# Kernel tuning notes

Measured on AMD Instinct MI355X. Metric: run time of the kernel, lower is better.

Reference implementation:

```python
import jax, jax.numpy as jnp
import numpy as np

N = 100000   # nodes
E = 1600000  # edges
IN, HID, OUT = 128, 128, 64


def setup_inputs() -> dict:
    key = jax.random.key(0)
    ks = jax.random.split(key, 8)
    x = jax.random.normal(ks[0], (N, IN), dtype=jnp.float32)
    edge_index = jax.random.randint(ks[1], (2, E), 0, N, dtype=jnp.int64)
    W1 = jax.random.normal(ks[2], (IN, HID), dtype=jnp.float32) * 0.05
    b1 = jnp.zeros((HID,), dtype=jnp.float32)
    W2 = jax.random.normal(ks[3], (HID, OUT), dtype=jnp.float32) * 0.05
    b2 = jnp.zeros((OUT,), dtype=jnp.float32)
    Wd = jax.random.normal(ks[4], (OUT, IN), dtype=jnp.float32) * 0.05
    bd = jnp.zeros((IN,), dtype=jnp.float32)
    return {"x": x, "edge_index": edge_index, "W1": W1, "b1": b1,
            "W2": W2, "b2": b2, "Wd": Wd, "bd": bd}


def _gcn_conv(x, src, dst, W, b):
    # PyG GCNConv: add self-loops, symmetric normalization D^-1/2 (A+I) D^-1/2,
    # messages flow src -> dst, aggregated by sum at dst.
    h = x @ W                                   # [N, F]
    ones = jnp.ones((src.shape[0],), x.dtype)
    deg = jax.ops.segment_sum(ones, dst, num_segments=N) + 1.0  # +1 for self-loop
    dinv = jax.lax.rsqrt(deg)                   # deg^-1/2, [N]
    coef = dinv[src] * dinv[dst]                # per-edge norm
    agg = jax.ops.segment_sum(h[src] * coef[:, None], dst, num_segments=N)
    agg = agg + h * (dinv * dinv)[:, None]      # self-loop contribution
    return agg + b


def reference(x, edge_index, W1, b1, W2, b2, Wd, bd):
    src, dst = edge_index[0], edge_index[1]
    h = jax.nn.relu(_gcn_conv(x, src, dst, W1, b1))
    # dropout in eval mode -> identity
    z = _gcn_conv(h, src, dst, W2, b2)          # [N, OUT] embedding
    x_recon = z @ Wd + bd                        # [N, IN]
    return (x_recon, z)
```

## Files before the change

### kernel.cpp

```cpp
#include <hip/hip_runtime.h>
#include <hip/hip_bf16.h>
#include <hip/hip_fp16.h>


#define TPB 256
#define CAP 64

typedef float v2f __attribute__((ext_vector_type(2)));


__device__ __forceinline__ unsigned short f2bf(float f) {
    unsigned u = __float_as_uint(f);
    unsigned r = u + 0x7fffu + ((u >> 16) & 1u);
    return (unsigned short)(r >> 16);
}
__device__ __forceinline__ float bf_lo(unsigned u) { return __uint_as_float(u << 16); }
__device__ __forceinline__ float bf_hi(unsigned u) { return __uint_as_float(u & 0xffff0000u); }


template <int K, int C, int TN, bool BIAS, bool INBF, bool OUTBF>
__device__ __forceinline__ void gemm_body(const void* __restrict__ Ap,
                                          const float* __restrict__ W,
                                          const float* __restrict__ bias,
                                          void* __restrict__ outp, int N, int bid,
                                          float* __restrict__ Ws) {
    constexpr int BM  = 128;
    constexpr int TM  = 8;
    constexpr int BK  = 32;
    constexpr int NCT = C / TN;
    static_assert(NCT * (BM / TM) == TPB, "thread layout");

    int tid = threadIdx.x;
    int tc = tid % NCT;
    int tr = tid / NCT;
    int c0 = tc * TN;
    int r0 = bid * BM + tr * TM;

    float acc[TM][TN] = {};

    for (int k0 = 0; k0 < K; k0 += BK) {
        __syncthreads();
        for (int i = tid * 4; i < BK * C; i += TPB * 4)
            *(float4*)&Ws[i] = *(const float4*)&W[k0 * C + i];
        __syncthreads();

        for (int k = 0; k < BK; k += 4) {
            float4 a[TM];
            uint2  au[TM];
#pragma unroll
            for (int i = 0; i < TM; ++i) {
                int r = r0 + i;
                if (r >= N) r = N - 1;
                if (INBF)
                    au[i] = *(const uint2*)((const unsigned short*)Ap + (size_t)r * K + k0 + k);
                else
                    a[i] = *(const float4*)((const float*)Ap + (size_t)r * K + k0 + k);
            }
#pragma unroll
            for (int kk = 0; kk < 4; ++kk) {
                float w[TN];
#pragma unroll
                for (int j = 0; j < TN; j += 4)
                    *(float4*)&w[j] = *(const float4*)&Ws[(k + kk) * C + c0 + j];
#pragma unroll
                for (int i = 0; i < TM; ++i) {
                    float av;
                    if (INBF) {
                        unsigned uu = (kk < 2) ? au[i].x : au[i].y;
                        av = (kk & 1) ? bf_hi(uu) : bf_lo(uu);
                    } else {
                        av = ((const float*)&a[i])[kk];
                    }
#pragma unroll
                    for (int j = 0; j < TN; ++j) acc[i][j] += av * w[j];
                }
            }
        }
    }

#pragma unroll
    for (int i = 0; i < TM; ++i) {
        int r = r0 + i;
        if (r >= N) continue;
        if (BIAS) {
#pragma unroll
            for (int j = 0; j < TN; ++j) acc[i][j] += bias[c0 + j];
        }
        if (OUTBF) {
            unsigned short* ob = (unsigned short*)outp + (size_t)r * C + c0;
            unsigned pk[TN / 2];
#pragma unroll
            for (int j = 0; j < TN; j += 2)
                pk[j / 2] = (unsigned)f2bf(acc[i][j]) | ((unsigned)f2bf(acc[i][j + 1]) << 16);
            if (TN == 8)      *(uint4*)ob = *(uint4*)pk;
            else if (TN == 4) *(uint2*)ob = *(uint2*)pk;
        } else {
            float* of = (float*)outp + (size_t)r * C + c0;
#pragma unroll
            for (int j = 0; j < TN; j += 4)
                *(float4*)&of[j] = *(float4*)&acc[i][j];
        }
    }
}

template <int K, int C, int TN, bool BIAS, bool INBF, bool OUTBF>
__global__ __launch_bounds__(TPB) void gemm_k(const void* __restrict__ Ap,
                                              const float* __restrict__ W,
                                              const float* __restrict__ bias,
                                              void* __restrict__ outp, int N) {
    __shared__ float Ws[32 * C];
    gemm_body<K, C, TN, BIAS, INBF, OUTBF>(Ap, W, bias, outp, N, blockIdx.x, Ws);
}


__global__ __launch_bounds__(TPB) void fused1_k(const float* __restrict__ x,
                                                const float* __restrict__ W1,
                                                unsigned* __restrict__ h1b,
                                                const int* __restrict__ src,
                                                const int* __restrict__ dst,
                                                int* __restrict__ cnt,
                                                unsigned* __restrict__ bucket,
                                                int N, int E, int gb) {
    __shared__ float Ws[32 * 128];
    if ((int)blockIdx.x < gb) {
        gemm_body<128, 128, 8, false, false, true>(x, W1, nullptr, h1b, N, blockIdx.x, Ws);
    } else {
        int bid = (int)blockIdx.x - gb;
        int e0 = (bid * TPB + (int)threadIdx.x) * 8;
        if (e0 + 7 < E) {
            int4 sa = *(const int4*)&src[e0];
            int4 sb = *(const int4*)&src[e0 + 4];
            int4 da = *(const int4*)&dst[e0];
            int4 db = *(const int4*)&dst[e0 + 4];
            int ss[8] = {sa.x, sa.y, sa.z, sa.w, sb.x, sb.y, sb.z, sb.w};
            int dd[8] = {da.x, da.y, da.z, da.w, db.x, db.y, db.z, db.w};
            int rr[8];
#pragma unroll
            for (int q = 0; q < 8; ++q) rr[q] = atomicAdd(&cnt[dd[q]], 1);
#pragma unroll
            for (int q = 0; q < 8; ++q)
                if (rr[q] < CAP) bucket[(size_t)rr[q] * N + dd[q]] = (unsigned)ss[q];
        } else {
            for (int e = e0; e < E; ++e) {
                int s = src[e], d = dst[e];
                int r = atomicAdd(&cnt[d], 1);
                if (r < CAP) bucket[(size_t)r * N + d] = (unsigned)s;
            }
        }
    }
}


template <int F2, bool RELU, bool OUTBF>
__global__ __launch_bounds__(TPB) void agg_k(const unsigned* __restrict__ h,
                                             const int* __restrict__ cnt,
                                             const unsigned* __restrict__ bucket,
                                             const float* __restrict__ bias,
                                             void* __restrict__ outp, int N) {
    constexpr int NPB = TPB / F2;
    int ln = threadIdx.x / F2;
    int f2 = threadIdx.x % F2;
    int n  = blockIdx.x * NPB + ln;
    if (n >= N) return;

    int cfull = cnt[n];
    float di = rsqrtf((float)cfull + 1.0f);
    unsigned us = h[(size_t)n * F2 + f2];
    float ax = bf_lo(us) * (di * di);
    float ay = bf_hi(us) * (di * di);

    int cn = cfull < CAP ? cfull : CAP;
    const unsigned* bp = bucket + n;

    int j = 0;
    for (; j + 7 < cn; j += 8) {
        int s[8], cs[8];
        unsigned v[8];
#pragma unroll
        for (int q = 0; q < 8; ++q) s[q] = (int)bp[(size_t)(j + q) * N];
#pragma unroll
        for (int q = 0; q < 8; ++q) {
            v[q]  = h[(size_t)s[q] * F2 + f2];
            cs[q] = cnt[s[q]];
        }
#pragma unroll
        for (int q = 0; q < 8; ++q) {
            float c = rsqrtf((float)cs[q] + 1.0f) * di;
            ax += c * bf_lo(v[q]);
            ay += c * bf_hi(v[q]);
        }
    }
    for (; j < cn; ++j) {
        int s = (int)bp[(size_t)j * N];
        unsigned v = h[(size_t)s * F2 + f2];
        float c = rsqrtf((float)cnt[s] + 1.0f) * di;
        ax += c * bf_lo(v);
        ay += c * bf_hi(v);
    }

    float rx = ax + bias[2 * f2];
    float ry = ay + bias[2 * f2 + 1];
    if (RELU) { rx = fmaxf(rx, 0.f); ry = fmaxf(ry, 0.f); }
    if (OUTBF) {
        unsigned pk = (unsigned)f2bf(rx) | ((unsigned)f2bf(ry) << 16);
        ((unsigned*)outp)[(size_t)n * F2 + f2] = pk;
    } else {
        v2f r; r.x = rx; r.y = ry;
        __builtin_nontemporal_store(r, (v2f*)outp + (size_t)n * F2 + f2);
    }
}


extern "C" void kernel_launch(void* const* d_in, const int* in_sizes, int n_in,
                              void* d_out, int out_size, void* d_ws, size_t ws_size,
                              hipStream_t stream) {
    const float* x    = (const float*)d_in[0];
    const int*   eidx = (const int*)d_in[1];
    const float* W1   = (const float*)d_in[2];
    const float* b1   = (const float*)d_in[3];
    const float* W2   = (const float*)d_in[4];
    const float* b2   = (const float*)d_in[5];
    const float* Wd   = (const float*)d_in[6];
    const float* bd   = (const float*)d_in[7];

    const int N = in_sizes[0] / 128;
    const int E = in_sizes[1] / 2;
    const int* src = eidx;
    const int* dst = eidx + E;

    size_t off = 0;
    auto alloc = [&](size_t bytes) {
        void* p = (char*)d_ws + off;
        off += (bytes + 255) & ~(size_t)255;
        return p;
    };
    int*      cnt     = (int*)alloc((size_t)N * 4);
    unsigned* bucket  = (unsigned*)alloc((size_t)N * CAP * 4);
    unsigned* h1b     = (unsigned*)alloc((size_t)N * 64 * 4);
    unsigned* h2b     = (unsigned*)alloc((size_t)N * 32 * 4);
    unsigned* hrelu_b = (unsigned*)alloc((size_t)N * 64 * 4);
    (void)ws_size;

    float* x_recon = (float*)d_out;
    float* z_out   = (float*)d_out + (size_t)N * 128;

    const int gb = (N + 127) / 128;
    const int fb = (E + TPB * 8 - 1) / (TPB * 8);

    (void)hipMemsetAsync(cnt, 0, (size_t)N * 4, stream);

    fused1_k<<<gb + fb, TPB, 0, stream>>>(x, W1, h1b, src, dst, cnt, bucket, N, E, gb);

    agg_k<64, true, true><<<(N + 3) / 4, TPB, 0, stream>>>(h1b, cnt, bucket, b1, hrelu_b, N);
    gemm_k<128, 64, 4, false, true, true><<<gb, TPB, 0, stream>>>(hrelu_b, W2, nullptr, h2b, N);
    agg_k<32, false, false><<<(N + 7) / 8, TPB, 0, stream>>>(h2b, cnt, bucket, b2, z_out, N);
    gemm_k<64, 128, 8, true, false, false><<<gb, TPB, 0, stream>>>(z_out, Wd, bd, x_recon, N);
}
```

Before: 475.1 us.

## Pre-partition edges into destination-range bins before bucket fill

Edges are first binned into 8 destination-range bins, using a block-local histogram and one global atomic per bin, and written to a scratch buffer that reuses the hrelu workspace. A new fill kernel then walks each bin and does the cnt atomics and bucket scatter, so concurrent writes from a bin land in a narrower address range. The aim is better cache locality for the atomic counters and scattered bucket writes. It costs an extra kernel launch and a write and read of the binned edge list, and bins are capped at BINCAP, so edges could be dropped if a bin overflows.

```diff
diff --git a/kernel.cpp b/kernel.cpp
--- a/kernel.cpp
+++ b/kernel.cpp
@@ -5,6 +5,8 @@
 
 #define TPB 256
 #define CAP 64
+#define BINCAP 220000
+#define FILLW 112
 
 typedef float v2f __attribute__((ext_vector_type(2)));
 
@@ -118,33 +120,82 @@
                                                 unsigned* __restrict__ h1b,
                                                 const int* __restrict__ src,
                                                 const int* __restrict__ dst,
-                                                int* __restrict__ cnt,
-                                                unsigned* __restrict__ bucket,
-                                                int N, int E, int gb) {
+                                                uint2* __restrict__ binBuf,
+                                                int* __restrict__ binCnt,
+                                                int N, int E, int gb, unsigned M) {
     __shared__ float Ws[32 * 128];
+    __shared__ int hist[8], gbase[8], lpos[8];
     if ((int)blockIdx.x < gb) {
         gemm_body<128, 128, 8, false, false, true>(x, W1, nullptr, h1b, N, blockIdx.x, Ws);
     } else {
         int bid = (int)blockIdx.x - gb;
-        int e0 = (bid * TPB + (int)threadIdx.x) * 8;
-        if (e0 + 7 < E) {
+        int tid = (int)threadIdx.x;
+        if (tid < 8) { hist[tid] = 0; lpos[tid] = 0; }
+        __syncthreads();
+
+        int e0 = (bid * TPB + tid) * 8;
+        int ne = E - e0; ne = ne > 8 ? 8 : (ne < 0 ? 0 : ne);
+        int ss[8], dd[8], bb8[8];
+        if (ne == 8) {
             int4 sa = *(const int4*)&src[e0];
             int4 sb = *(const int4*)&src[e0 + 4];
             int4 da = *(const int4*)&dst[e0];
             int4 db = *(const int4*)&dst[e0 + 4];
-            int ss[8] = {sa.x, sa.y, sa.z, sa.w, sb.x, sb.y, sb.z, sb.w};
-            int dd[8] = {da.x, da.y, da.z, da.w, db.x, db.y, db.z, db.w};
+            ss[0]=sa.x; ss[1]=sa.y; ss[2]=sa.z; ss[3]=sa.w;
+            ss[4]=sb.x; ss[5]=sb.y; ss[6]=sb.z; ss[7]=sb.w;
+            dd[0]=da.x; dd[1]=da.y; dd[2]=da.z; dd[3]=da.w;
+            dd[4]=db.x; dd[5]=db.y; dd[6]=db.z; dd[7]=db.w;
+        } else {
+            for (int q = 0; q < ne; ++q) { ss[q] = src[e0 + q]; dd[q] = dst[e0 + q]; }
+        }
+        for (int q = 0; q < ne; ++q) {
+            bb8[q] = (int)(((unsigned long long)(unsigned)dd[q] * M) >> 32);
+            atomicAdd(&hist[bb8[q]], 1);
+        }
+        __syncthreads();
+        if (tid < 8) gbase[tid] = atomicAdd(&binCnt[tid], hist[tid]);
+        __syncthreads();
+        for (int q = 0; q < ne; ++q) {
+            int b = bb8[q];
+            int p = gbase[b] + atomicAdd(&lpos[b], 1);
+            if (p < BINCAP)
+                binBuf[(size_t)b * BINCAP + p] = make_uint2((unsigned)ss[q], (unsigned)dd[q]);
+        }
+    }
+}
+
+
+__global__ __launch_bounds__(TPB) void fill_k(const uint2* __restrict__ binBuf,
+                                              const int* __restrict__ binCnt,
+                                              int* __restrict__ cnt,
+                                              unsigned* __restrict__ bucket, int N) {
+    int bin = (int)blockIdx.x & 7;
+    int w   = (int)blockIdx.x >> 3;
+    int cb  = binCnt[bin];
+    if (cb > BINCAP) cb = BINCAP;
+    const uint2* eb = binBuf + (size_t)bin * BINCAP;
+
+    for (int base = w * (TPB * 8); base < cb; base += FILLW * (TPB * 8)) {
+        int e0 = base + (int)threadIdx.x * 8;
+        if (e0 + 8 <= cb) {
+            unsigned s[8], d[8];
+#pragma unroll
+            for (int q = 0; q < 8; q += 2) {
+                uint4 t = *(const uint4*)&eb[e0 + q];
+                s[q] = t.x; d[q] = t.y; s[q + 1] = t.z; d[q + 1] = t.w;
+            }
             int rr[8];
 #pragma unroll
-            for (int q = 0; q < 8; ++q) rr[q] = atomicAdd(&cnt[dd[q]], 1);
+            for (int q = 0; q < 8; ++q) rr[q] = atomicAdd(&cnt[(int)d[q]], 1);
 #pragma unroll
             for (int q = 0; q < 8; ++q)
-                if (rr[q] < CAP) bucket[(size_t)rr[q] * N + dd[q]] = (unsigned)ss[q];
+                if (rr[q] < CAP) bucket[(size_t)rr[q] * N + d[q]] = s[q];
         } else {
-            for (int e = e0; e < E; ++e) {
-                int s = src[e], d = dst[e];
-                int r = atomicAdd(&cnt[d], 1);
-                if (r < CAP) bucket[(size_t)r * N + d] = (unsigned)s;
+            int lim = e0 + 8 < cb ? e0 + 8 : cb;
+            for (int e = e0; e < lim; ++e) {
+                uint2 t = eb[e];
+                int r = atomicAdd(&cnt[(int)t.y], 1);
+                if (r < CAP) bucket[(size_t)r * N + t.y] = t.x;
             }
         }
     }
@@ -239,17 +290,22 @@
     unsigned* h1b     = (unsigned*)alloc((size_t)N * 64 * 4);
     unsigned* h2b     = (unsigned*)alloc((size_t)N * 32 * 4);
     unsigned* hrelu_b = (unsigned*)alloc((size_t)N * 64 * 4);
+    int*      binCnt  = (int*)alloc(256);
+    uint2*    binBuf  = (uint2*)hrelu_b;
     (void)ws_size;
 
     float* x_recon = (float*)d_out;
     float* z_out   = (float*)d_out + (size_t)N * 128;
 
     const int gb = (N + 127) / 128;
-    const int fb = (E + TPB * 8 - 1) / (TPB * 8);
+    const int bb = (E + TPB * 8 - 1) / (TPB * 8);
+    const unsigned M = (unsigned)((8ULL << 32) / (unsigned)N);
 
     (void)hipMemsetAsync(cnt, 0, (size_t)N * 4, stream);
-
-    fused1_k<<<gb + fb, TPB, 0, stream>>>(x, W1, h1b, src, dst, cnt, bucket, N, E, gb);
+    (void)hipMemsetAsync(binCnt, 0, 256, stream);
+
+    fused1_k<<<gb + bb, TPB, 0, stream>>>(x, W1, h1b, src, dst, binBuf, binCnt, N, E, gb, M);
+    fill_k<<<8 * FILLW, TPB, 0, stream>>>(binBuf, binCnt, cnt, bucket, N);
 
     agg_k<64, true, true><<<(N + 3) / 4, TPB, 0, stream>>>(h1b, cnt, bucket, b1, hrelu_b, N);
     gemm_k<128, 64, 4, false, true, true><<<gb, TPB, 0, stream>>>(hrelu_b, W2, nullptr, h2b, N);
```

Result: no change. 473.5 us (-0.3%).
